# Performance work log

Hardware: AMD Instinct MI355X
Metric: run time of the kernel (lower is better)

The kernel has to match this reference:

```python
import jax, jax.numpy as jnp
import numpy as np

B, S = 8, 2048
D_IN, D_STATE, D_OUT = 1024, 1024, 1024
H = 16
DH = D_STATE // H  # 64
N_LAYERS = 24
STD = 0.02
EPS = 1e-6


def setup_inputs() -> dict:
    key = jax.random.key(0)
    k = jax.random.split(key, 4)
    x = jax.random.normal(k[0], (B, S, D_IN), dtype=jnp.float32)
    # input_projection: Linear(D_IN, 4*D_STATE, bias=False), std=0.02
    w_in = jax.random.normal(k[1], (D_IN, 4 * D_STATE), dtype=jnp.float32) * STD
    # state_weight: [3*H, DH, DH] recurrence matrices (candidate, forget, reset)
    state_weight = jax.random.normal(k[2], (3 * H, DH, DH), dtype=jnp.float32) * STD
    # rmsnorm weight over state_size
    norm_weight = jnp.ones((D_STATE,), dtype=jnp.float32)
    # output_projection: Linear(D_STATE, D_OUT, bias=False), std scaled by sqrt(2*num_layers)
    w_out = jax.random.normal(k[3], (D_STATE, D_OUT), dtype=jnp.float32) * (STD / np.sqrt(2 * N_LAYERS))
    return {"x": x, "w_in": w_in, "state_weight": state_weight,
            "norm_weight": norm_weight, "w_out": w_out}


def _rmsnorm(x, w):
    var = jnp.mean(jnp.square(x), axis=-1, keepdims=True)
    return x * jax.lax.rsqrt(var + EPS) * w


def reference(x, w_in, state_weight, norm_weight, w_out):
    # input projection -> [B, S, 4*D_STATE]
    proj = jnp.einsum('bsi,io->bso', x, w_in)
    xg, g = jnp.split(proj, [3 * D_STATE], axis=-1)
    xi, xf, xr = jnp.split(xg, 3, axis=-1)
    # per-head views [B, S, H, DH]
    xi = xi.reshape(B, S, H, DH)
    xf = xf.reshape(B, S, H, DH)
    xr = xr.reshape(B, S, H, DH)
    W, Wf, Wr = jnp.split(state_weight, 3, axis=0)  # each [H, DH, DH]

    # scan over time: carry h [B, H, DH]
    def step(h, inp):
        xi_t, xf_t, xr_t = inp  # each [B, H, DH]
        r = jax.nn.sigmoid(xr_t + jnp.einsum('bhd,hde->bhe', h, Wr))
        f = jax.nn.sigmoid(xf_t + jnp.einsum('bhd,hde->bhe', h, Wf))
        c = jnp.tanh(xi_t + jnp.einsum('bhd,hde->bhe', r * h, W))
        h_new = f * h + (1.0 - f) * c
        return h_new, h_new

    h0 = jnp.zeros((B, H, DH), dtype=x.dtype)
    xs = (jnp.swapaxes(xi, 0, 1), jnp.swapaxes(xf, 0, 1), jnp.swapaxes(xr, 0, 1))
    _, hs = jax.lax.scan(step, h0, xs)  # hs: [S, B, H, DH]
    h_seq = jnp.swapaxes(hs, 0, 1).reshape(B, S, D_STATE)

    # gated output: h * silu(g), rmsnorm, output projection
    y = h_seq * jax.nn.silu(g)
    y = _rmsnorm(y, norm_weight)
    return jnp.einsum('bsd,do->bso', y, w_out)
```

## Files before the change

### kernel.cpp

```cpp
#include <hip/hip_runtime.h>
#include <hip/hip_bf16.h>
#include <math.h>

typedef __hip_bfloat16 bf16;

#define B_      8
#define S_      2048
#define DIN     1024
#define DSTATE  1024
#define H_      16
#define DH_     64
#define PROJ4   4096

#define BARRIER_LGKM() asm volatile("s_waitcnt lgkmcnt(0)\n\ts_barrier" ::: "memory")

__device__ __forceinline__ unsigned short f2bf(float f) {
    unsigned int x = __float_as_uint(f);
    x += 0x7FFFu + ((x >> 16) & 1u);
    return (unsigned short)(x >> 16);
}

__device__ __forceinline__ float4 load4(const float* p) { return *(const float4*)p; }
__device__ __forceinline__ float4 load4(const bf16* p) {
    uint2 u = *(const uint2*)p;
    float4 r;
    r.x = __uint_as_float((u.x & 0xFFFFu) << 16);
    r.y = __uint_as_float(u.x & 0xFFFF0000u);
    r.z = __uint_as_float((u.y & 0xFFFFu) << 16);
    r.w = __uint_as_float(u.y & 0xFFFF0000u);
    return r;
}
__device__ __forceinline__ void store4(float* p, float4 v) { *(float4*)p = v; }
__device__ __forceinline__ void store4(bf16* p, float4 v) {
    uint2 u;
    u.x = (unsigned int)f2bf(v.x) | ((unsigned int)f2bf(v.y) << 16);
    u.y = (unsigned int)f2bf(v.z) | ((unsigned int)f2bf(v.w) << 16);
    *(uint2*)p = u;
}

typedef __attribute__((ext_vector_type(8))) short bf16x8;
typedef __attribute__((ext_vector_type(4))) float f32x4;
typedef __attribute__((ext_vector_type(2))) float f32x2;
typedef __attribute__((ext_vector_type(4))) short short4v;

template <typename TA>
__device__ __forceinline__ void load_a4(const TA* p, float out[4]);
template <>
__device__ __forceinline__ void load_a4<float>(const float* p, float out[4]) {
    float4 v = *(const float4*)p;
    out[0] = v.x; out[1] = v.y; out[2] = v.z; out[3] = v.w;
}
template <>
__device__ __forceinline__ void load_a4<bf16>(const bf16* p, float out[4]) {
    float4 v = load4(p);
    out[0] = v.x; out[1] = v.y; out[2] = v.z; out[3] = v.w;
}

template <typename TA, typename TC>
__global__ __launch_bounds__(256) void gemm_mfma(const TA* __restrict__ A,
                                                 const float* __restrict__ Bm,
                                                 TC* __restrict__ C,
                                                 int M, int N, int K, int lda) {
    __shared__ short As[128][40];
    __shared__ short Bs[128][40];

    const int tid = threadIdx.x;
    const int m0 = blockIdx.y * 128;
    const int n0 = blockIdx.x * 128;

    const int saM = tid >> 1;
    const int saK = (tid & 1) * 16;
    const int sbK = tid >> 3;
    const int sbN = (tid & 7) * 16;

    const int wid = tid >> 6;
    const int wx = wid & 1, wy = wid >> 1;
    const int lane = tid & 63;
    const int c16 = lane & 15;
    const int quad = lane >> 4;

    const TA* Aptr = A + (size_t)(m0 + saM) * lda + saK;
    const float* Bptr = Bm + (size_t)sbK * N + n0 + sbN;

    f32x4 acc[4][4];
    #pragma unroll
    for (int i = 0; i < 4; ++i)
        #pragma unroll
        for (int j = 0; j < 4; ++j) acc[i][j] = (f32x4){0.f, 0.f, 0.f, 0.f};

    float ra[4][4];
    float rb[4][4];
    #pragma unroll
    for (int i = 0; i < 4; ++i) load_a4<TA>(Aptr + i * 4, ra[i]);
    #pragma unroll
    for (int i = 0; i < 4; ++i) {
        float4 v = load4(Bptr + i * 4);
        rb[i][0] = v.x; rb[i][1] = v.y; rb[i][2] = v.z; rb[i][3] = v.w;
    }

    for (int k0 = 0; k0 < K; k0 += 32) {
        __syncthreads();
        #pragma unroll
        for (int i = 0; i < 4; ++i) {
            short4v pk = { (short)f2bf(ra[i][0]), (short)f2bf(ra[i][1]),
                           (short)f2bf(ra[i][2]), (short)f2bf(ra[i][3]) };
            *(short4v*)&As[saM][saK + i * 4] = pk;
        }
        #pragma unroll
        for (int i = 0; i < 4; ++i)
            #pragma unroll
            for (int j = 0; j < 4; ++j)
                Bs[sbN + i * 4 + j][sbK] = (short)f2bf(rb[i][j]);
        __syncthreads();

        if (k0 + 32 < K) {
            #pragma unroll
            for (int i = 0; i < 4; ++i) load_a4<TA>(Aptr + k0 + 32 + i * 4, ra[i]);
            #pragma unroll
            for (int i = 0; i < 4; ++i) {
                float4 v = load4(Bptr + (size_t)(k0 + 32) * N + i * 4);
                rb[i][0] = v.x; rb[i][1] = v.y; rb[i][2] = v.z; rb[i][3] = v.w;
            }
        }

        bf16x8 af[4], bfr[4];
        #pragma unroll
        for (int mt = 0; mt < 4; ++mt)
            af[mt] = *(const bf16x8*)&As[wy * 64 + mt * 16 + c16][quad * 8];
        #pragma unroll
        for (int nt = 0; nt < 4; ++nt)
            bfr[nt] = *(const bf16x8*)&Bs[wx * 64 + nt * 16 + c16][quad * 8];

        #pragma unroll
        for (int mt = 0; mt < 4; ++mt)
            #pragma unroll
            for (int nt = 0; nt < 4; ++nt)
                acc[mt][nt] = __builtin_amdgcn_mfma_f32_16x16x32_bf16(
                    af[mt], bfr[nt], acc[mt][nt], 0, 0, 0);
    }

    #pragma unroll
    for (int mt = 0; mt < 4; ++mt) {
        #pragma unroll
        for (int r = 0; r < 4; ++r) {
            int row = m0 + wy * 64 + mt * 16 + quad * 4 + r;
            TC* cp = C + (size_t)row * N + n0 + wx * 64;
            #pragma unroll
            for (int nt = 0; nt < 4; ++nt)
                cp[nt * 16 + c16] = (TC)acc[mt][nt][r];
        }
    }
}

__device__ __forceinline__ float lane_bcast(float v, int lane) {
    return __int_as_float(__builtin_amdgcn_readlane(__float_as_int(v), lane));
}

#define RPT16(M) M(0) M(1) M(2) M(3) M(4) M(5) M(6) M(7) \
                 M(8) M(9) M(10) M(11) M(12) M(13) M(14) M(15)

__global__ __launch_bounds__(256, 1)
__attribute__((amdgpu_waves_per_eu(1, 2)))
void recur_kernel(bf16* __restrict__ proj, const float* __restrict__ sw) {
    const int tid = threadIdx.x;
    const int e = tid & 63;
    const int w = __builtin_amdgcn_readfirstlane(tid >> 6);
    const int d0 = w << 4;
    const int bh = blockIdx.x;
    const int b = bh >> 4;
    const int h = bh & 15;

    __shared__ float2 part_rf[4][64];
    __shared__ float  part_c[4][64];

    __shared__ char lds_force[60 * 1024];
    asm volatile("" :: "v"((unsigned int)(size_t)lds_force));

    const float* Wc_p = sw + (size_t)h * 4096 + (size_t)d0 * 64 + e;
    const float* Wf_p = Wc_p + (size_t)16 * 4096;
    const float* Wr_p = Wc_p + (size_t)32 * 4096;

    #define DECLW(i) float wc##i, wf##i, wr##i;
    RPT16(DECLW)
    #undef DECLW
    #define LOADW(i) wc##i = Wc_p[(i) * 64]; \
                     wf##i = Wf_p[(i) * 64]; \
                     wr##i = Wr_p[(i) * 64];
    RPT16(LOADW)
    #undef LOADW
    #define PINW(i) asm volatile("" : "+v"(wc##i), "+v"(wf##i), "+v"(wr##i));
    RPT16(PINW)
    #undef PINW

    bf16* xi_p = proj + (size_t)b * S_ * PROJ4 + h * 64 + e;

    f32x4 rxi, rxf, rxr;
    #define PRELOAD(U) { const bf16* p = xi_p + (size_t)(U) * PROJ4; \
        rxi[U] = __bfloat162float(p[0]); \
        rxf[U] = __bfloat162float(p[1024]); \
        rxr[U] = __bfloat162float(p[2048]); }
    PRELOAD(0) PRELOAD(1) PRELOAD(2) PRELOAD(3)
    #undef PRELOAD

    float hreg = 0.0f;

    const bf16* ld = xi_p + (size_t)4 * PROJ4;
    bf16*       st = xi_p;

    #define P1T(i, A) { float hb = lane_bcast(hreg, d0 + (i)); \
        aR##A = fmaf(hb, wr##i, aR##A); \
        aF##A = fmaf(hb, wf##i, aF##A); }
    #define P2T(i, A) { float qb = lane_bcast(rh, d0 + (i)); \
        aC##A = fmaf(qb, wc##i, aC##A); }

    #define STEP(U, REFILL) { \
        float xi0 = rxi[U], xf0 = rxf[U], xr0 = rxr[U]; \
        if (REFILL) { \
            const bf16* p = ld + (size_t)(U) * PROJ4; \
            rxi[U] = __bfloat162float(p[0]); \
            rxf[U] = __bfloat162float(p[1024]); \
            rxr[U] = __bfloat162float(p[2048]); \
        } \
        float aR0 = 0.f, aR1 = 0.f, aF0 = 0.f, aF1 = 0.f; \
        P1T(0,0)  P1T(1,1)  P1T(2,0)  P1T(3,1) \
        P1T(4,0)  P1T(5,1)  P1T(6,0)  P1T(7,1) \
        P1T(8,0)  P1T(9,1)  P1T(10,0) P1T(11,1) \
        P1T(12,0) P1T(13,1) P1T(14,0) P1T(15,1) \
        part_rf[w][e] = make_float2(aR0 + aR1, aF0 + aF1); \
        BARRIER_LGKM(); \
        float2 p0 = part_rf[0][e], p1 = part_rf[1][e]; \
        float2 p2 = part_rf[2][e], p3 = part_rf[3][e]; \
        float sr = xr0 + (p0.x + p1.x) + (p2.x + p3.x); \
        float sf = xf0 + (p0.y + p1.y) + (p2.y + p3.y); \
        float r = 1.f / (1.f + __expf(-sr)); \
        float f = 1.f / (1.f + __expf(-sf)); \
        float rh = r * hreg; \
        float aC0 = 0.f, aC1 = 0.f; \
        P2T(0,0)  P2T(1,1)  P2T(2,0)  P2T(3,1) \
        P2T(4,0)  P2T(5,1)  P2T(6,0)  P2T(7,1) \
        P2T(8,0)  P2T(9,1)  P2T(10,0) P2T(11,1) \
        P2T(12,0) P2T(13,1) P2T(14,0) P2T(15,1) \
        part_c[w][e] = aC0 + aC1; \
        BARRIER_LGKM(); \
        float sc = xi0 + (part_c[0][e] + part_c[1][e]) \
                       + (part_c[2][e] + part_c[3][e]); \
        sc = fminf(fmaxf(sc, -15.f), 15.f); \
        float ex = __expf(-2.f * sc); \
        float cc = (1.f - ex) / (1.f + ex); \
        hreg = f * hreg + (1.f - f) * cc; \
        if (w == (U)) st[(size_t)(U) * PROJ4] = __float2bfloat16(hreg); \
    }

    for (int t0 = 0; t0 < S_ - 4; t0 += 4) {
        STEP(0, 1) STEP(1, 1) STEP(2, 1) STEP(3, 1)
        ld += (size_t)4 * PROJ4;
        st += (size_t)4 * PROJ4;
    }
    STEP(0, 0) STEP(1, 0) STEP(2, 0) STEP(3, 0)

    #undef STEP
    #undef P1T
    #undef P2T
}

__global__ __launch_bounds__(256) void gate_norm_kernel(bf16* __restrict__ proj,
                                                        const float* __restrict__ nw) {
    const int row = blockIdx.x;
    const int tid = threadIdx.x;
    __shared__ float red[4];

    bf16* hp = proj + (size_t)row * PROJ4;
    const bf16* gp = hp + 3 * DSTATE;

    float4 hv = load4(hp + tid * 4);
    float4 gv = load4(gp + tid * 4);

    float v0 = hv.x * (gv.x / (1.f + __expf(-gv.x)));
    float v1 = hv.y * (gv.y / (1.f + __expf(-gv.y)));
    float v2 = hv.z * (gv.z / (1.f + __expf(-gv.z)));
    float v3 = hv.w * (gv.w / (1.f + __expf(-gv.w)));

    float ss = v0 * v0 + v1 * v1 + v2 * v2 + v3 * v3;
    #pragma unroll
    for (int mask = 32; mask >= 1; mask >>= 1)
        ss += __shfl_xor(ss, mask, 64);

    const int wid = tid >> 6;
    if ((tid & 63) == 0) red[wid] = ss;
    __syncthreads();
    float tot = red[0] + red[1] + red[2] + red[3];
    float scale = rsqrtf(tot * (1.0f / (float)DSTATE) + 1e-6f);

    float4 nv = *(const float4*)(nw + tid * 4);
    float4 y;
    y.x = v0 * scale * nv.x;
    y.y = v1 * scale * nv.y;
    y.z = v2 * scale * nv.z;
    y.w = v3 * scale * nv.w;
    store4(hp + tid * 4, y);
}

extern "C" void kernel_launch(void* const* d_in, const int* in_sizes, int n_in,
                              void* d_out, int out_size, void* d_ws, size_t ws_size,
                              hipStream_t stream) {
    const float* x     = (const float*)d_in[0];
    const float* w_in  = (const float*)d_in[1];
    const float* sw    = (const float*)d_in[2];
    const float* nw    = (const float*)d_in[3];
    const float* w_out = (const float*)d_in[4];
    float* out = (float*)d_out;

    bf16* proj = (bf16*)d_ws;

    dim3 g1(PROJ4 / 128, (B_ * S_) / 128);
    gemm_mfma<float, bf16><<<g1, 256, 0, stream>>>(x, w_in, proj,
                                                   B_ * S_, PROJ4, DIN, DIN);

    recur_kernel<<<128, 256, 0, stream>>>(proj, sw);

    gate_norm_kernel<<<B_ * S_, 256, 0, stream>>>(proj, nw);

    dim3 g2(DSTATE / 128, (B_ * S_) / 128);
    gemm_mfma<bf16, float><<<g2, 256, 0, stream>>>(proj, w_out, out,
                                                   B_ * S_, DSTATE, DSTATE, PROJ4);
}
```

Baseline: 1.709 ms.

## Pre-cast inputs to bf16 and pre-transpose weights for simpler GEMM staging

Adds a cast kernel that converts x to bf16 and a transpose-cast kernel that stores both weight matrices as bf16 in N-major order. Both GEMMs then run a new kernel that stages A and B tiles with straight 16-byte copies into LDS, with no per-element conversion and no scattered transposed LDS stores. This is meant to cut conversion ALU work and LDS bank conflicts in the GEMM inner loop. In exchange it adds three extra launches and an extra read and write pass over x (64 MB in, 32 MB out) plus the weights each call.

```diff
diff --git a/kernel.cpp b/kernel.cpp
--- a/kernel.cpp
+++ b/kernel.cpp
@@ -40,38 +40,62 @@
 
 typedef __attribute__((ext_vector_type(8))) short bf16x8;
 typedef __attribute__((ext_vector_type(4))) float f32x4;
-typedef __attribute__((ext_vector_type(2))) float f32x2;
-typedef __attribute__((ext_vector_type(4))) short short4v;
-
-template <typename TA>
-__device__ __forceinline__ void load_a4(const TA* p, float out[4]);
-template <>
-__device__ __forceinline__ void load_a4<float>(const float* p, float out[4]) {
-    float4 v = *(const float4*)p;
-    out[0] = v.x; out[1] = v.y; out[2] = v.z; out[3] = v.w;
-}
-template <>
-__device__ __forceinline__ void load_a4<bf16>(const bf16* p, float out[4]) {
-    float4 v = load4(p);
-    out[0] = v.x; out[1] = v.y; out[2] = v.z; out[3] = v.w;
-}
-
-template <typename TA, typename TC>
-__global__ __launch_bounds__(256) void gemm_mfma(const TA* __restrict__ A,
-                                                 const float* __restrict__ Bm,
-                                                 TC* __restrict__ C,
-                                                 int M, int N, int K, int lda) {
-    __shared__ short As[128][40];
-    __shared__ short Bs[128][40];
+
+__global__ __launch_bounds__(256) void cast_x_kernel(const float* __restrict__ src,
+                                                     bf16* __restrict__ dst, int n8) {
+    int i = blockIdx.x * 256 + threadIdx.x;
+    if (i >= n8) return;
+    const float* p = src + (size_t)i * 8;
+    bf16* q = dst + (size_t)i * 8;
+    store4(q, load4(p));
+    store4(q + 4, load4(p + 4));
+}
+
+__global__ __launch_bounds__(256) void transpose_cast_kernel(
+        const float* __restrict__ src, bf16* __restrict__ dst, int R, int C) {
+    __shared__ short t64[64][65];
+    const int tid = threadIdx.x;
+    const int r0 = blockIdx.y * 64;
+    const int c0 = blockIdx.x * 64;
+    const int rr = tid >> 4;
+    const int c4 = (tid & 15) * 4;
+
+    #pragma unroll
+    for (int p = 0; p < 4; ++p) {
+        int r = rr + p * 16;
+        float4 v = load4(src + (size_t)(r0 + r) * C + c0 + c4);
+        t64[r][c4 + 0] = (short)f2bf(v.x);
+        t64[r][c4 + 1] = (short)f2bf(v.y);
+        t64[r][c4 + 2] = (short)f2bf(v.z);
+        t64[r][c4 + 3] = (short)f2bf(v.w);
+    }
+    __syncthreads();
+    #pragma unroll
+    for (int p = 0; p < 4; ++p) {
+        int cc = rr + p * 16;
+        unsigned int s0 = (unsigned short)t64[c4 + 0][cc] |
+                          ((unsigned int)(unsigned short)t64[c4 + 1][cc] << 16);
+        unsigned int s1 = (unsigned short)t64[c4 + 2][cc] |
+                          ((unsigned int)(unsigned short)t64[c4 + 3][cc] << 16);
+        uint2 u = make_uint2(s0, s1);
+        *(uint2*)&dst[(size_t)(c0 + cc) * R + r0 + c4] = u;
+    }
+}
+
+template <typename TC>
+__global__ __launch_bounds__(256) void gemm_bt(const bf16* __restrict__ A,
+                                               const bf16* __restrict__ BT,
+                                               TC* __restrict__ C,
+                                               int N, int K, int lda, int ldb) {
+    __shared__ short As[128 * 40];
+    __shared__ short Bs[128 * 40];
 
     const int tid = threadIdx.x;
     const int m0 = blockIdx.y * 128;
     const int n0 = blockIdx.x * 128;
 
-    const int saM = tid >> 1;
-    const int saK = (tid & 1) * 16;
-    const int sbK = tid >> 3;
-    const int sbN = (tid & 7) * 16;
+    const int row = tid >> 1;
+    const int ks  = (tid & 1) * 16;
 
     const int wid = tid >> 6;
     const int wx = wid & 1, wy = wid >> 1;
@@ -79,8 +103,8 @@
     const int c16 = lane & 15;
     const int quad = lane >> 4;
 
-    const TA* Aptr = A + (size_t)(m0 + saM) * lda + saK;
-    const float* Bptr = Bm + (size_t)sbK * N + n0 + sbN;
+    const bf16* Ap = A + (size_t)(m0 + row) * lda + ks;
+    const bf16* Bp = BT + (size_t)(n0 + row) * ldb + ks;
 
     f32x4 acc[4][4];
     #pragma unroll
@@ -88,48 +112,33 @@
         #pragma unroll
         for (int j = 0; j < 4; ++j) acc[i][j] = (f32x4){0.f, 0.f, 0.f, 0.f};
 
-    float ra[4][4];
-    float rb[4][4];
-    #pragma unroll
-    for (int i = 0; i < 4; ++i) load_a4<TA>(Aptr + i * 4, ra[i]);
-    #pragma unroll
-    for (int i = 0; i < 4; ++i) {
-        float4 v = load4(Bptr + i * 4);
-        rb[i][0] = v.x; rb[i][1] = v.y; rb[i][2] = v.z; rb[i][3] = v.w;
-    }
+    uint4 ra0 = *(const uint4*)Ap;
+    uint4 ra1 = *(const uint4*)(Ap + 8);
+    uint4 rb0 = *(const uint4*)Bp;
+    uint4 rb1 = *(const uint4*)(Bp + 8);
 
     for (int k0 = 0; k0 < K; k0 += 32) {
         __syncthreads();
-        #pragma unroll
-        for (int i = 0; i < 4; ++i) {
-            short4v pk = { (short)f2bf(ra[i][0]), (short)f2bf(ra[i][1]),
-                           (short)f2bf(ra[i][2]), (short)f2bf(ra[i][3]) };
-            *(short4v*)&As[saM][saK + i * 4] = pk;
+        *(uint4*)&As[row * 40 + ks]     = ra0;
+        *(uint4*)&As[row * 40 + ks + 8] = ra1;
+        *(uint4*)&Bs[row * 40 + ks]     = rb0;
+        *(uint4*)&Bs[row * 40 + ks + 8] = rb1;
+        __syncthreads();
+
+        if (k0 + 32 < K) {
+            ra0 = *(const uint4*)(Ap + k0 + 32);
+            ra1 = *(const uint4*)(Ap + k0 + 40);
+            rb0 = *(const uint4*)(Bp + k0 + 32);
+            rb1 = *(const uint4*)(Bp + k0 + 40);
         }
-        #pragma unroll
-        for (int i = 0; i < 4; ++i)
-            #pragma unroll
-            for (int j = 0; j < 4; ++j)
-                Bs[sbN + i * 4 + j][sbK] = (short)f2bf(rb[i][j]);
-        __syncthreads();
-
-        if (k0 + 32 < K) {
-            #pragma unroll
-            for (int i = 0; i < 4; ++i) load_a4<TA>(Aptr + k0 + 32 + i * 4, ra[i]);
-            #pragma unroll
-            for (int i = 0; i < 4; ++i) {
-                float4 v = load4(Bptr + (size_t)(k0 + 32) * N + i * 4);
-                rb[i][0] = v.x; rb[i][1] = v.y; rb[i][2] = v.z; rb[i][3] = v.w;
-            }
-        }
 
         bf16x8 af[4], bfr[4];
         #pragma unroll
         for (int mt = 0; mt < 4; ++mt)
-            af[mt] = *(const bf16x8*)&As[wy * 64 + mt * 16 + c16][quad * 8];
+            af[mt] = *(const bf16x8*)&As[(wy * 64 + mt * 16 + c16) * 40 + quad * 8];
         #pragma unroll
         for (int nt = 0; nt < 4; ++nt)
-            bfr[nt] = *(const bf16x8*)&Bs[wx * 64 + nt * 16 + c16][quad * 8];
+            bfr[nt] = *(const bf16x8*)&Bs[(wx * 64 + nt * 16 + c16) * 40 + quad * 8];
 
         #pragma unroll
         for (int mt = 0; mt < 4; ++mt)
@@ -143,8 +152,8 @@
     for (int mt = 0; mt < 4; ++mt) {
         #pragma unroll
         for (int r = 0; r < 4; ++r) {
-            int row = m0 + wy * 64 + mt * 16 + quad * 4 + r;
-            TC* cp = C + (size_t)row * N + n0 + wx * 64;
+            int rowc = m0 + wy * 64 + mt * 16 + quad * 4 + r;
+            TC* cp = C + (size_t)rowc * N + n0 + wx * 64;
             #pragma unroll
             for (int nt = 0; nt < 4; ++nt)
                 cp[nt * 16 + c16] = (TC)acc[mt][nt][r];
@@ -172,7 +181,6 @@
 
     __shared__ float2 part_rf[4][64];
     __shared__ float  part_c[4][64];
-
     __shared__ char lds_force[60 * 1024];
     asm volatile("" :: "v"((unsigned int)(size_t)lds_force));
 
@@ -310,17 +318,26 @@
     const float* w_out = (const float*)d_in[4];
     float* out = (float*)d_out;
 
-    bf16* proj = (bf16*)d_ws;
-
-    dim3 g1(PROJ4 / 128, (B_ * S_) / 128);
-    gemm_mfma<float, bf16><<<g1, 256, 0, stream>>>(x, w_in, proj,
-                                                   B_ * S_, PROJ4, DIN, DIN);
+    char* ws = (char*)d_ws;
+    bf16* proj   = (bf16*)ws;
+    bf16* xb     = (bf16*)(ws + 134217728);
+    bf16* w_inT  = (bf16*)(ws + 134217728 + 33554432);
+    bf16* w_outT = (bf16*)(ws + 134217728 + 33554432 + 8388608);
+
+    cast_x_kernel<<<(B_ * S_ * DIN / 8 + 255) / 256, 256, 0, stream>>>(x, xb,
+                                                                B_ * S_ * DIN / 8);
+    transpose_cast_kernel<<<dim3(PROJ4 / 64, DIN / 64), 256, 0, stream>>>(
+        w_in, w_inT, DIN, PROJ4);
+    transpose_cast_kernel<<<dim3(DSTATE / 64, DSTATE / 64), 256, 0, stream>>>(
+        w_out, w_outT, DSTATE, DSTATE);
+
+    gemm_bt<bf16><<<dim3(PROJ4 / 128, (B_ * S_) / 128), 256, 0, stream>>>(
+        xb, w_inT, proj, PROJ4, DIN, DIN, DIN);
 
     recur_kernel<<<128, 256, 0, stream>>>(proj, sw);
 
     gate_norm_kernel<<<B_ * S_, 256, 0, stream>>>(proj, nw);
 
-    dim3 g2(DSTATE / 128, (B_ * S_) / 128);
-    gemm_mfma<bf16, float><<<g2, 256, 0, stream>>>(proj, w_out, out,
-                                                   B_ * S_, DSTATE, DSTATE, PROJ4);
-}
+    gemm_bt<float><<<dim3(DSTATE / 128, (B_ * S_) / 128), 256, 0, stream>>>(
+        proj, w_outT, out, DSTATE, DSTATE, PROJ4, DSTATE);
+}
```

Measured after the change: 1.482 ms. 13.3% less time.
